# Kernel optimization log

Measured on AMD Instinct MI355X. Metric: run time of the kernel, lower is better.

The kernel has to match this reference:

```python
import jax, jax.numpy as jnp
import numpy as np

N_NODES = 50000
N_EDGES = 800000
D_IN = 128
D_OUT = 128


def setup_inputs() -> dict:
    key = jax.random.key(0)
    k1, k2, k3, k4, k5 = jax.random.split(key, 5)
    gain = float(np.sqrt(2.0))  # calculate_gain('relu')
    # xavier_uniform bound: gain * sqrt(6/(fan_in+fan_out))
    bound = gain * float(np.sqrt(6.0 / (D_IN + D_OUT)))
    feat = jax.random.normal(k1, (N_NODES, D_IN), dtype=jnp.float32)
    weight = jax.random.uniform(k2, (D_IN, D_OUT), minval=-bound, maxval=bound, dtype=jnp.float32)
    loop_weight = jax.random.uniform(k3, (D_IN, D_OUT), minval=-bound, maxval=bound, dtype=jnp.float32)
    h_bias = jnp.zeros((D_OUT,), dtype=jnp.float32)
    src = jax.random.randint(k4, (N_EDGES,), 0, N_NODES, dtype=jnp.int32)
    dst = jax.random.randint(k5, (N_EDGES,), 0, N_NODES, dtype=jnp.int32)
    return {"feat": feat, "weight": weight, "h_bias": h_bias,
            "loop_weight": loop_weight, "src": src, "dst": dst}


def reference(feat, weight, h_bias, loop_weight, src, dst):
    # message: m_e = feat[src_e] @ W ; aggregate: h_v = sum_{e: dst_e=v} m_e
    # (equivalently transform-then-gather, which avoids the [E, D] matmul)
    transformed = feat @ weight                    # [N, D_out]
    msgs = transformed[src]                        # [E, D_out] gather
    h = jax.ops.segment_sum(msgs, dst, num_segments=feat.shape[0])  # [N, D_out]
    h = h + h_bias                                 # bias
    h = h + feat @ loop_weight                     # self-loop
    # activation=None, dropout=0 -> identity
    return h
```

## Files before the change

### kernel.cpp

```cpp
#include <hip/hip_runtime.h>

#define D 128
#define CAP 64
#define FCHUNK 2048

typedef __attribute__((ext_vector_type(8))) short bf16x8;
typedef __attribute__((ext_vector_type(4))) float f32x4;

__device__ inline unsigned short f2bf_rne(float x) {
    unsigned u = __float_as_uint(x);
    return (unsigned short)((u + 0x7FFFu + ((u >> 16) & 1u)) >> 16);
}

__global__ __launch_bounds__(256) void prep_kernel(
    const float* __restrict__ W, const float* __restrict__ LW,
    unsigned short* __restrict__ Bt, int* __restrict__ cursor, int N)
{
    int tid = blockIdx.x * 256 + threadIdx.x;
    if (tid < 2 * D * D) {
        int n = tid >> 7;
        int k = tid & 127;
        float v = (n < D) ? W[(size_t)k * D + n] : LW[(size_t)k * D + (n - D)];
        Bt[(size_t)n * D + k] = f2bf_rne(v);
    }
    int j = tid - 2 * D * D;
    if (j >= 0 && j < N) cursor[j] = 0;
}

__global__ __launch_bounds__(256) void merged_kernel(
    const float* __restrict__ feat, const unsigned short* __restrict__ Bt,
    unsigned short* __restrict__ T2,
    const int* __restrict__ src, const int* __restrict__ dst,
    int* __restrict__ cursor, unsigned short* __restrict__ ebuf,
    int N, int E, int gb_mfma)
{
    if ((int)blockIdx.x < gb_mfma) {
        const int wave = threadIdx.x >> 6;
        const int lane = threadIdx.x & 63;
        const int row0 = blockIdx.x * 16;
        const int m    = lane & 15;
        const int kg   = lane >> 4;

        int arow_idx = row0 + m;
        if (arow_idx >= N) arow_idx = N - 1;
        const float* arow = feat + (size_t)arow_idx * D;

        bf16x8 a[4];
#pragma unroll
        for (int ks = 0; ks < 4; ++ks) {
            const float4 f0 = *(const float4*)(arow + ks * 32 + kg * 8);
            const float4 f1 = *(const float4*)(arow + ks * 32 + kg * 8 + 4);
            bf16x8 v;
            v[0] = (short)f2bf_rne(f0.x); v[1] = (short)f2bf_rne(f0.y);
            v[2] = (short)f2bf_rne(f0.z); v[3] = (short)f2bf_rne(f0.w);
            v[4] = (short)f2bf_rne(f1.x); v[5] = (short)f2bf_rne(f1.y);
            v[6] = (short)f2bf_rne(f1.z); v[7] = (short)f2bf_rne(f1.w);
            a[ks] = v;
        }

        const int colbase = wave * 64;
        f32x4 acc[4];
#pragma unroll
        for (int t = 0; t < 4; ++t) acc[t] = (f32x4){0.f, 0.f, 0.f, 0.f};

#pragma unroll
        for (int t = 0; t < 4; ++t) {
            const unsigned short* brow = Bt + (size_t)(colbase + t * 16 + m) * D;
#pragma unroll
            for (int ks = 0; ks < 4; ++ks) {
                bf16x8 b = *(const bf16x8*)(brow + ks * 32 + kg * 8);
                acc[t] = __builtin_amdgcn_mfma_f32_16x16x32_bf16(a[ks], b, acc[t], 0, 0, 0);
            }
        }

#pragma unroll
        for (int t = 0; t < 4; ++t) {
            const int col = colbase + t * 16 + m;
#pragma unroll
            for (int r = 0; r < 4; ++r) {
                const int row = row0 + kg * 4 + r;
                if (row < N) T2[(size_t)row * 256 + col] = f2bf_rne(acc[t][r]);
            }
        }
    } else {
        const int fb    = (int)blockIdx.x - gb_mfma;
        const int chunk = fb >> 3;
        const int cls   = (int)blockIdx.x & 7;
        const int base  = chunk * FCHUNK;

        for (int i = threadIdx.x; i < FCHUNK; i += 256) {
            const int e = base + i;
            if (e >= E) break;
            const int d = dst[e];
            if ((d & 7) == cls) {
                int pos = atomicAdd(&cursor[d], 1);
                if (pos < CAP) ebuf[(size_t)d * CAP + pos] = (unsigned short)src[e];
            }
        }
    }
}

__global__ __launch_bounds__(256) void gather_kernel(
    const unsigned short* __restrict__ ebuf, const int* __restrict__ cursor,
    const unsigned short* __restrict__ T2, const float* __restrict__ bias,
    float* __restrict__ out, int N)
{
    const int node = (blockIdx.x * 256 + threadIdx.x) >> 6;
    const int lane = threadIdx.x & 63;
    if (node >= N) return;

    int deg = cursor[node];
    if (deg > CAP) deg = CAP;

    const unsigned* region = (const unsigned*)(ebuf + (size_t)node * CAP);
    const unsigned short* Tbase = T2 + 2 * lane;

    float ax = 0.f, ay = 0.f;

    for (int j = 0; j < deg; j += 8) {
        unsigned w[4];
#pragma unroll
        for (int k = 0; k < 4; ++k) w[k] = region[(j >> 1) + k];

        unsigned u[8];
#pragma unroll
        for (int k = 0; k < 8; ++k) {
            const unsigned s = (k & 1) ? (w[k >> 1] >> 16) : (w[k >> 1] & 0xFFFFu);
            u[k] = *(const unsigned*)(Tbase + (size_t)s * 256);
        }
#pragma unroll
        for (int k = 0; k < 8; ++k) {
            const bool live = (j + k) < deg;
            ax += live ? __uint_as_float(u[k] << 16) : 0.f;
            ay += live ? __uint_as_float(u[k] & 0xFFFF0000u) : 0.f;
        }
    }

    const unsigned sw = *(const unsigned*)(T2 + (size_t)node * 256 + 128 + 2 * lane);
    const float2 b = *(const float2*)(bias + 2 * lane);
    float2 o;
    o.x = b.x + __uint_as_float(sw << 16) + ax;
    o.y = b.y + __uint_as_float(sw & 0xFFFF0000u) + ay;
    *(float2*)(out + (size_t)node * D + 2 * lane) = o;
}

extern "C" void kernel_launch(void* const* d_in, const int* in_sizes, int n_in,
                              void* d_out, int out_size, void* d_ws, size_t ws_size,
                              hipStream_t stream) {
    const float* feat = (const float*)d_in[0];
    const float* W    = (const float*)d_in[1];
    const float* bias = (const float*)d_in[2];
    const float* LW   = (const float*)d_in[3];
    const int*   src  = (const int*)d_in[4];
    const int*   dst  = (const int*)d_in[5];
    float* out = (float*)d_out;

    const int N = in_sizes[0] / D;
    const int E = in_sizes[4];

    unsigned short* T2   = (unsigned short*)d_ws;
    unsigned short* Bt   = T2 + (size_t)N * 256;
    unsigned short* ebuf = Bt + 2 * D * D;
    int* cursor = (int*)(ebuf + (size_t)N * CAP);

    {
        const int work = 2 * D * D + N;
        prep_kernel<<<dim3((work + 255) / 256), 256, 0, stream>>>(W, LW, Bt, cursor, N);
    }

    {
        const int gb_mfma = (N + 15) / 16;
        const int nchunks = (E + FCHUNK - 1) / FCHUNK;
        merged_kernel<<<dim3(gb_mfma + nchunks * 8), 256, 0, stream>>>(
            feat, Bt, T2, src, dst, cursor, ebuf, N, E, gb_mfma);
    }

    gather_kernel<<<dim3((N + 3) / 4), 256, 0, stream>>>(ebuf, cursor, T2, bias, out, N);
}
```

Measured before the change: 189.0 us.

## Split merged MFMA/fill kernel, class-partition cursor array, enlarge fill chunks

Splits the merged kernel into a separate edge-bucketing fill kernel and an MFMA transform kernel, launched back to back. The per-node cursor array is re-laid out so that each destination class (d & 7) owns a contiguous range, which concentrates each fill block's atomics in a smaller region. The fill chunk size is doubled so fewer blocks each process more edges, and src is now loaded unconditionally alongside dst. Running the two kernels in sequence gives up the overlap of GEMM and bucketing in exchange for less heterogeneous blocks and better atomic locality.

Result: no change. 190.9 us (+1.0%).

```diff
diff --git a/kernel.cpp b/kernel.cpp
--- a/kernel.cpp
+++ b/kernel.cpp
@@ -2,7 +2,7 @@
 
 #define D 128
 #define CAP 64
-#define FCHUNK 2048
+#define FCHUNK 4096
 
 typedef __attribute__((ext_vector_type(8))) short bf16x8;
 typedef __attribute__((ext_vector_type(4))) float f32x4;
@@ -12,9 +12,13 @@
     return (unsigned short)((u + 0x7FFFu + ((u >> 16) & 1u)) >> 16);
 }
 
+__device__ __host__ inline int cidx(int d, int cstride) {
+    return (d & 7) * cstride + (d >> 3);
+}
+
 __global__ __launch_bounds__(256) void prep_kernel(
     const float* __restrict__ W, const float* __restrict__ LW,
-    unsigned short* __restrict__ Bt, int* __restrict__ cursor, int N)
+    unsigned short* __restrict__ Bt, int* __restrict__ cursor, int ncur)
 {
     int tid = blockIdx.x * 256 + threadIdx.x;
     if (tid < 2 * D * D) {
@@ -24,78 +28,79 @@
         Bt[(size_t)n * D + k] = f2bf_rne(v);
     }
     int j = tid - 2 * D * D;
-    if (j >= 0 && j < N) cursor[j] = 0;
+    if (j >= 0 && j < ncur) cursor[j] = 0;
 }
 
-__global__ __launch_bounds__(256) void merged_kernel(
-    const float* __restrict__ feat, const unsigned short* __restrict__ Bt,
-    unsigned short* __restrict__ T2,
+__global__ __launch_bounds__(256) void fill_kernel(
     const int* __restrict__ src, const int* __restrict__ dst,
     int* __restrict__ cursor, unsigned short* __restrict__ ebuf,
-    int N, int E, int gb_mfma)
+    int E, int cstride)
 {
-    if ((int)blockIdx.x < gb_mfma) {
-        const int wave = threadIdx.x >> 6;
-        const int lane = threadIdx.x & 63;
-        const int row0 = blockIdx.x * 16;
-        const int m    = lane & 15;
-        const int kg   = lane >> 4;
+    const int chunk = blockIdx.x >> 3;
+    const int cls   = blockIdx.x & 7;
+    const int base  = chunk * FCHUNK;
 
-        int arow_idx = row0 + m;
-        if (arow_idx >= N) arow_idx = N - 1;
-        const float* arow = feat + (size_t)arow_idx * D;
+    for (int i = threadIdx.x; i < FCHUNK; i += 256) {
+        const int e = base + i;
+        if (e >= E) break;
+        const int d = dst[e];
+        const int s = src[e];
+        if ((d & 7) == cls) {
+            int pos = atomicAdd(&cursor[(cls * cstride) + (d >> 3)], 1);
+            if (pos < CAP) ebuf[(size_t)d * CAP + pos] = (unsigned short)s;
+        }
+    }
+}
 
-        bf16x8 a[4];
+__global__ __launch_bounds__(256) void mfma_transform(
+    const float* __restrict__ feat, const unsigned short* __restrict__ Bt,
+    unsigned short* __restrict__ T2, int N)
+{
+    const int wave = threadIdx.x >> 6;
+    const int lane = threadIdx.x & 63;
+    const int row0 = blockIdx.x * 16;
+    const int m    = lane & 15;
+    const int kg   = lane >> 4;
+
+    int arow_idx = row0 + m;
+    if (arow_idx >= N) arow_idx = N - 1;
+    const float* arow = feat + (size_t)arow_idx * D;
+
+    bf16x8 a[4];
+#pragma unroll
+    for (int ks = 0; ks < 4; ++ks) {
+        const float4 f0 = *(const float4*)(arow + ks * 32 + kg * 8);
+        const float4 f1 = *(const float4*)(arow + ks * 32 + kg * 8 + 4);
+        bf16x8 v;
+        v[0] = (short)f2bf_rne(f0.x); v[1] = (short)f2bf_rne(f0.y);
+        v[2] = (short)f2bf_rne(f0.z); v[3] = (short)f2bf_rne(f0.w);
+        v[4] = (short)f2bf_rne(f1.x); v[5] = (short)f2bf_rne(f1.y);
+        v[6] = (short)f2bf_rne(f1.z); v[7] = (short)f2bf_rne(f1.w);
+        a[ks] = v;
+    }
+
+    const int colbase = wave * 64;
+    f32x4 acc[4];
+#pragma unroll
+    for (int t = 0; t < 4; ++t) acc[t] = (f32x4){0.f, 0.f, 0.f, 0.f};
+
+#pragma unroll
+    for (int t = 0; t < 4; ++t) {
+        const unsigned short* brow = Bt + (size_t)(colbase + t * 16 + m) * D;
 #pragma unroll
         for (int ks = 0; ks < 4; ++ks) {
-            const float4 f0 = *(const float4*)(arow + ks * 32 + kg * 8);
-            const float4 f1 = *(const float4*)(arow + ks * 32 + kg * 8 + 4);
-            bf16x8 v;
-            v[0] = (short)f2bf_rne(f0.x); v[1] = (short)f2bf_rne(f0.y);
-            v[2] = (short)f2bf_rne(f0.z); v[3] = (short)f2bf_rne(f0.w);
-            v[4] = (short)f2bf_rne(f1.x); v[5] = (short)f2bf_rne(f1.y);
-            v[6] = (short)f2bf_rne(f1.z); v[7] = (short)f2bf_rne(f1.w);
-            a[ks] = v;
+            bf16x8 b = *(const bf16x8*)(brow + ks * 32 + kg * 8);
+            acc[t] = __builtin_amdgcn_mfma_f32_16x16x32_bf16(a[ks], b, acc[t], 0, 0, 0);
         }
-
-        const int colbase = wave * 64;
-        f32x4 acc[4];
-#pragma unroll
-        for (int t = 0; t < 4; ++t) acc[t] = (f32x4){0.f, 0.f, 0.f, 0.f};
+    }
 
 #pragma unroll
-        for (int t = 0; t < 4; ++t) {
-            const unsigned short* brow = Bt + (size_t)(colbase + t * 16 + m) * D;
+    for (int t = 0; t < 4; ++t) {
+        const int col = colbase + t * 16 + m;
 #pragma unroll
-            for (int ks = 0; ks < 4; ++ks) {
-                bf16x8 b = *(const bf16x8*)(brow + ks * 32 + kg * 8);
-                acc[t] = __builtin_amdgcn_mfma_f32_16x16x32_bf16(a[ks], b, acc[t], 0, 0, 0);
-            }
-        }
-
-#pragma unroll
-        for (int t = 0; t < 4; ++t) {
-            const int col = colbase + t * 16 + m;
-#pragma unroll
-            for (int r = 0; r < 4; ++r) {
-                const int row = row0 + kg * 4 + r;
-                if (row < N) T2[(size_t)row * 256 + col] = f2bf_rne(acc[t][r]);
-            }
-        }
-    } else {
-        const int fb    = (int)blockIdx.x - gb_mfma;
-        const int chunk = fb >> 3;
-        const int cls   = (int)blockIdx.x & 7;
-        const int base  = chunk * FCHUNK;
-
-        for (int i = threadIdx.x; i < FCHUNK; i += 256) {
-            const int e = base + i;
-            if (e >= E) break;
-            const int d = dst[e];
-            if ((d & 7) == cls) {
-                int pos = atomicAdd(&cursor[d], 1);
-                if (pos < CAP) ebuf[(size_t)d * CAP + pos] = (unsigned short)src[e];
-            }
+        for (int r = 0; r < 4; ++r) {
+            const int row = row0 + kg * 4 + r;
+            if (row < N) T2[(size_t)row * 256 + col] = f2bf_rne(acc[t][r]);
         }
     }
 }
@@ -103,13 +108,13 @@
 __global__ __launch_bounds__(256) void gather_kernel(
     const unsigned short* __restrict__ ebuf, const int* __restrict__ cursor,
     const unsigned short* __restrict__ T2, const float* __restrict__ bias,
-    float* __restrict__ out, int N)
+    float* __restrict__ out, int N, int cstride)
 {
     const int node = (blockIdx.x * 256 + threadIdx.x) >> 6;
     const int lane = threadIdx.x & 63;
     if (node >= N) return;
 
-    int deg = cursor[node];
+    int deg = cursor[((node & 7) * cstride) + (node >> 3)];
     if (deg > CAP) deg = CAP;
 
     const unsigned* region = (const unsigned*)(ebuf + (size_t)node * CAP);
@@ -157,6 +162,8 @@
 
     const int N = in_sizes[0] / D;
     const int E = in_sizes[4];
+    const int cstride = (N + 7) >> 3;
+    const int ncur = 8 * cstride;
 
     unsigned short* T2   = (unsigned short*)d_ws;
     unsigned short* Bt   = T2 + (size_t)N * 256;
@@ -164,16 +171,16 @@
     int* cursor = (int*)(ebuf + (size_t)N * CAP);
 
     {
-        const int work = 2 * D * D + N;
-        prep_kernel<<<dim3((work + 255) / 256), 256, 0, stream>>>(W, LW, Bt, cursor, N);
+        const int work = 2 * D * D + ncur;
+        prep_kernel<<<dim3((work + 255) / 256), 256, 0, stream>>>(W, LW, Bt, cursor, ncur);
     }
 
     {
-        const int gb_mfma = (N + 15) / 16;
         const int nchunks = (E + FCHUNK - 1) / FCHUNK;
-        merged_kernel<<<dim3(gb_mfma + nchunks * 8), 256, 0, stream>>>(
-            feat, Bt, T2, src, dst, cursor, ebuf, N, E, gb_mfma);
+        fill_kernel<<<dim3(nchunks * 8), 256, 0, stream>>>(src, dst, cursor, ebuf, E, cstride);
     }
 
-    gather_kernel<<<dim3((N + 3) / 4), 256, 0, stream>>>(ebuf, cursor, T2, bias, out, N);
+    mfma_transform<<<dim3((N + 15) / 16), 256, 0, stream>>>(feat, Bt, T2, N);
+
+    gather_kernel<<<dim3((N + 3) / 4), 256, 0, stream>>>(ebuf, cursor, T2, bias, out, N, cstride);
 }
```
